# Optimization experiments

Hardware: AMD Instinct MI355X
Metric: run time of the kernel (lower is better)

## Reference

```python
import jax, jax.numpy as jnp
import numpy as np

B, M, S, D, Q, H = 8, 8192, 128, 512, 32, 8
HD = D // H
LN_EPS = 1e-5


def setup_inputs() -> dict:
    key = jax.random.key(0)
    ks = jax.random.split(key, 12)
    inp = {
        "memory": jax.random.normal(ks[0], (B, M, D), dtype=jnp.float32),
        "context": jax.random.normal(ks[1], (B, S, D), dtype=jnp.float32),
        "memory_mask": jax.random.randint(ks[2], (B, M), 0, 2).astype(bool),
        # learned parameters
        "queries_param": jax.random.normal(ks[3], (Q, D), dtype=jnp.float32) * 0.02,
        "ctx_w": jax.random.normal(ks[4], (D, D), dtype=jnp.float32) / np.sqrt(D),
        "ctx_b": jnp.zeros((D,), dtype=jnp.float32),
        "in_w": jax.random.normal(ks[5], (3 * D, D), dtype=jnp.float32) / np.sqrt(D),
        "in_b": jnp.zeros((3 * D,), dtype=jnp.float32),
        "out_w": jax.random.normal(ks[6], (D, D), dtype=jnp.float32) / np.sqrt(D),
        "out_b": jnp.zeros((D,), dtype=jnp.float32),
        "ln_g": jnp.ones((D,), dtype=jnp.float32),
        "ln_b": jnp.zeros((D,), dtype=jnp.float32),
        "gate_w": jax.random.normal(ks[7], (Q, D), dtype=jnp.float32) / np.sqrt(D),
        "gate_b": jnp.zeros((Q,), dtype=jnp.float32),
    }
    return inp


def _forward(memory, context, memory_mask, queries_param, ctx_w, ctx_b,
             in_w, in_b, out_w, out_b, ln_g, ln_b, gate_w, gate_b):
    b = memory.shape[0]
    # pool context over sequence dim (rank-3 path)
    pooled = context.mean(axis=1)  # [B, D]
    # queries + projected context
    queries = queries_param[None, :, :] + (pooled @ ctx_w.T + ctx_b)[:, None, :]  # [B, Q, D]
    # MultiheadAttention in-projection
    wq, wk, wv = in_w[:D], in_w[D:2 * D], in_w[2 * D:]
    bq, bk, bv = in_b[:D], in_b[D:2 * D], in_b[2 * D:]
    qh = (queries @ wq.T + bq).reshape(b, Q, H, HD).transpose(0, 2, 1, 3)   # [B,H,Q,hd]
    kh = (memory @ wk.T + bk).reshape(b, M, H, HD).transpose(0, 2, 1, 3)    # [B,H,M,hd]
    vh = (memory @ wv.T + bv).reshape(b, M, H, HD).transpose(0, 2, 1, 3)    # [B,H,M,hd]
    scale = 1.0 / np.sqrt(HD)
    scores = jnp.einsum('bhqd,bhkd->bhqk', qh * scale, kh)                  # [B,H,Q,M]
    # key_padding_mask: True in memory_mask means valid; invalid -> -inf
    scores = jnp.where(memory_mask[:, None, None, :], scores, -jnp.inf)
    attn = jax.nn.softmax(scores, axis=-1)                                   # [B,H,Q,M]
    ctx_out = jnp.einsum('bhqk,bhkd->bhqd', attn, vh)
    ctx_out = ctx_out.transpose(0, 2, 1, 3).reshape(b, Q, D)
    readouts = ctx_out @ out_w.T + out_b                                     # [B,Q,D]
    attention = attn.mean(axis=1)                                            # [B,Q,M]
    gates = jax.nn.sigmoid(pooled @ gate_w.T + gate_b)                       # [B,Q]
    readouts = readouts * gates[:, :, None]
    mu = readouts.mean(axis=-1, keepdims=True)
    var = readouts.var(axis=-1, keepdims=True)
    readouts_norm = (readouts - mu) * jax.lax.rsqrt(var + LN_EPS) * ln_g + ln_b
    return readouts_norm, attention, gates, queries


def reference(memory, context, memory_mask, queries_param, ctx_w, ctx_b,
              in_w, in_b, out_w, out_b, ln_g, ln_b, gate_w, gate_b):
    return _forward(memory, context, memory_mask, queries_param, ctx_w, ctx_b,
                    in_w, in_b, out_w, out_b, ln_g, ln_b, gate_w, gate_b)
```

## Files before the change

kernel.cpp:

```cpp
#include <hip/hip_runtime.h>
#include <cstdint>

#define BB 8
#define MM 8192
#define SS 128
#define DD 512
#define QQ 32
#define HH 8
#define HDD 64
#define LN_EPS 1e-5f

typedef __bf16 bf16;
typedef _Float16 f16;
typedef __attribute__((ext_vector_type(8))) __bf16 bf16x8;
typedef __attribute__((ext_vector_type(4))) __bf16 bf16x4;
typedef __attribute__((ext_vector_type(8))) _Float16 f16x8;
typedef __attribute__((ext_vector_type(4))) float f32x4;

#define NEG_INF (-__builtin_inff())

__global__ __launch_bounds__(512) void k_front(const float* __restrict__ ctx,
                                               const float* __restrict__ ctx_w,
                                               const float* __restrict__ ctx_b,
                                               const float* __restrict__ qp,
                                               const float* __restrict__ gate_w,
                                               const float* __restrict__ gate_b,
                                               float* __restrict__ q_out,
                                               float* __restrict__ gates_out) {
    __shared__ float pl[DD];
    __shared__ float scratch[512];
    __shared__ float proj[64];
    int blk = blockIdx.x;
    int b = blk >> 3, js = blk & 7;
    int t = threadIdx.x;
    const float* p = ctx + (size_t)b * SS * DD + t;
    float s = 0.f;
#pragma unroll 8
    for (int i = 0; i < SS; i++) s += p[(size_t)i * DD];
    pl[t] = s * (1.0f / SS);
    __syncthreads();
    int r = js * 64 + (t & 63), ks = t >> 6;
    {
        const f32x4* wr = (const f32x4*)(ctx_w + (size_t)r * DD + ks * 64);
        const f32x4* pv = (const f32x4*)(pl + ks * 64);
        float a = 0.f;
#pragma unroll
        for (int k = 0; k < 16; k++) {
            f32x4 w = wr[k], pp = pv[k];
            a += w.x * pp.x + w.y * pp.y + w.z * pp.z + w.w * pp.w;
        }
        scratch[t] = a;
    }
    __syncthreads();
    if (t < 64) {
        float sum = ctx_b[js * 64 + t];
#pragma unroll
        for (int s8 = 0; s8 < 8; s8++) sum += scratch[t + 64 * s8];
        proj[t] = sum;
    }
    __syncthreads();
    int col = js * 64 + (t & 63);
    float pr = proj[t & 63];
#pragma unroll
    for (int qq = 0; qq < 4; qq++) {
        int q = (t >> 6) * 4 + qq;
        q_out[((size_t)(b * QQ + q)) * DD + col] = qp[q * DD + col] + pr;
    }
    if (js == 0 && t < QQ) {
        const f32x4* gw = (const f32x4*)(gate_w + (size_t)t * DD);
        const f32x4* pv = (const f32x4*)pl;
        float ga = 0.f;
#pragma unroll 8
        for (int k = 0; k < DD / 4; k++) {
            f32x4 w = gw[k], pp = pv[k];
            ga += w.x * pp.x + w.y * pp.y + w.z * pp.z + w.w * pp.w;
        }
        gates_out[b * QQ + t] = 1.0f / (1.0f + __expf(-(ga + gate_b[t])));
    }
}

__global__ __launch_bounds__(256) void k_qh(const float* __restrict__ q_in,
                                            const float* __restrict__ in_w,
                                            const float* __restrict__ in_b,
                                            float* __restrict__ qh) {
    __shared__ float qr[QQ * DD];
    int blk = blockIdx.x;
    int b = blk >> 3, js = blk & 7;
    int t = threadIdx.x;
    const f32x4* src = (const f32x4*)(q_in + (size_t)b * QQ * DD);
    f32x4* dst = (f32x4*)qr;
    for (int i = t; i < QQ * DD / 4; i += 256) dst[i] = src[i];
    __syncthreads();
    int j = js * 64 + (t & 63);
    int qg = t >> 6;
    const f32x4* wv = (const f32x4*)(in_w + (size_t)j * DD);
    float acc[8];
#pragma unroll
    for (int e = 0; e < 8; e++) acc[e] = 0.f;
    for (int k = 0; k < DD / 4; k++) {
        f32x4 w = wv[k];
#pragma unroll
        for (int e = 0; e < 8; e++) {
            f32x4 qq = ((const f32x4*)qr)[(qg * 8 + e) * (DD / 4) + k];
            acc[e] += w.x * qq.x + w.y * qq.y + w.z * qq.z + w.w * qq.w;
        }
    }
    float bias = in_b[j];
#pragma unroll
    for (int e = 0; e < 8; e++) {
        int q = qg * 8 + e;
        qh[((size_t)(b * QQ + q)) * DD + j] = 0.125f * (acc[e] + bias);
    }
}

#define N4_MEM 8388608
#define N4_W   131072
__global__ __launch_bounds__(256) void k_cvt2(const float* __restrict__ mem,
                                              const float* __restrict__ wsrc,
                                              bf16* __restrict__ memB,
                                              bf16* __restrict__ kvwB) {
    int stride = gridDim.x * blockDim.x;
    for (int i = blockIdx.x * blockDim.x + threadIdx.x; i < N4_MEM + N4_W; i += stride) {
        if (i < N4_MEM) {
            f32x4 v = ((const f32x4*)mem)[i];
            bf16x4 o;
            o.x = (bf16)v.x; o.y = (bf16)v.y; o.z = (bf16)v.z; o.w = (bf16)v.w;
            ((bf16x4*)memB)[i] = o;
        } else {
            int j = i - N4_MEM;
            f32x4 v = ((const f32x4*)wsrc)[j];
            bf16x4 o;
            o.x = (bf16)v.x; o.y = (bf16)v.y; o.z = (bf16)v.z; o.w = (bf16)v.w;
            ((bf16x4*)kvwB)[j] = o;
        }
    }
}

#define GLOAD(gp, lp)                                                                   \
    __builtin_amdgcn_global_load_lds((const __attribute__((address_space(1))) void*)(gp), \
                                     (__attribute__((address_space(3))) void*)(lp), 16, 0, 0)

__global__ __launch_bounds__(512, 2) void k_gemm_kv(const bf16* __restrict__ A,
                                                    const bf16* __restrict__ Bw,
                                                    const float* __restrict__ in_b,
                                                    bf16* __restrict__ Kh,
                                                    f16* __restrict__ Vt) {
    __shared__ __align__(16) bf16 sm[65536];
    const int tid = threadIdx.x;
    const int w = tid >> 6, l = tid & 63;
    const int wm = w >> 2, wn = w & 3;
    const int lq = l & 15, quad = l >> 4, lx = l & 7;
    const int lr = l >> 3, gc = (l & 7) ^ lr;
    const int sb = (w >> 1) * 8 + (w & 1) * 2;

    const int bid = blockIdx.x;
    const int swz = (bid & 7) * 128 + (bid >> 3);
    const int bm = swz >> 2, bn = swz & 3;

    const bf16* aPtr = A + (size_t)(bm * 256 + w * 8 + lr) * 512 + gc * 8;
    const bf16* bPtr = Bw + (size_t)(bn * 256 + sb * 8 + lr) * 512 + gc * 8;

#pragma unroll
    for (int p = 0; p < 4; p++) GLOAD(aPtr + p * 32768, sm + (p * 8 + w) * 512);
#pragma unroll
    for (int p = 0; p < 4; p++) {
        GLOAD(bPtr + ((p & 1) * 8 + (p >> 1) * 32) * 512,
              sm + 16384 + (sb + (p & 1) + (p >> 1) * 4) * 512);
        if (p == 1) __builtin_amdgcn_sched_barrier(0);
    }
    aPtr += 64;
    bPtr += 64;

    const f32x4 vzero = {0.f, 0.f, 0.f, 0.f};
    f32x4 acc[8][4];
#pragma unroll
    for (int i = 0; i < 8; i++)
#pragma unroll
        for (int j = 0; j < 4; j++) acc[i][j] = vzero;

#pragma unroll
    for (int T = 0; T < 8; T++) {
        bf16* Ab = sm + (T & 1) * 32768;
        bf16* Bb = Ab + 16384;
        bf16* AbN = sm + ((T + 1) & 1) * 32768;
        bf16* BbN = AbN + 16384;
        const bool pf = (T < 7);

        asm volatile("s_waitcnt vmcnt(2)" ::: "memory");
        __builtin_amdgcn_s_barrier();
        bf16x8 af[8][2], b01[2][2];
        {
            const int c0 = (quad ^ lx) << 3;
#pragma unroll
            for (int i = 0; i < 8; i++) {
                const bf16* rp = Ab + (wm * 128 + i * 16 + lq) * 64;
                af[i][0] = *(const bf16x8*)(rp + c0);
                af[i][1] = *(const bf16x8*)(rp + (c0 ^ 32));
            }
#pragma unroll
            for (int j = 0; j < 2; j++) {
                const bf16* rp = Bb + (wn * 64 + j * 16 + lq) * 64;
                b01[j][0] = *(const bf16x8*)(rp + c0);
                b01[j][1] = *(const bf16x8*)(rp + (c0 ^ 32));
            }
        }
        if (pf) {
#pragma unroll
            for (int p = 0; p < 4; p++) GLOAD(aPtr + p * 32768, AbN + (p * 8 + w) * 512);
            aPtr += 64;
        }
        __builtin_amdgcn_s_setprio(1);
#pragma unroll
        for (int i = 0; i < 8; i++)
#pragma unroll
            for (int j = 0; j < 2; j++) {
                acc[i][j] = __builtin_amdgcn_mfma_f32_16x16x32_bf16(af[i][0], b01[j][0], acc[i][j], 0, 0, 0);
                acc[i][j] = __builtin_amdgcn_mfma_f32_16x16x32_bf16(af[i][1], b01[j][1], acc[i][j], 0, 0, 0);
            }
        __builtin_amdgcn_s_setprio(0);

        if (pf) {
            asm volatile("s_waitcnt vmcnt(4)" ::: "memory");
        } else {
            asm volatile("s_waitcnt vmcnt(0)" ::: "memory");
        }
        __builtin_amdgcn_s_barrier();
        bf16x8 b23[2][2];
        {
            const int c0 = (quad ^ lx) << 3;
#pragma unroll
            for (int j = 0; j < 2; j++) {
                const bf16* rp = Bb + (wn * 64 + 32 + j * 16 + lq) * 64;
                b23[j][0] = *(const bf16x8*)(rp + c0);
                b23[j][1] = *(const bf16x8*)(rp + (c0 ^ 32));
            }
        }
        if (pf) {
#pragma unroll
            for (int p = 0; p < 4; p++) {
                GLOAD(bPtr + ((p & 1) * 8 + (p >> 1) * 32) * 512,
                      BbN + (sb + (p & 1) + (p >> 1) * 4) * 512);
                if (p == 1) __builtin_amdgcn_sched_barrier(0);
            }
            bPtr += 64;
        }
        __builtin_amdgcn_s_setprio(1);
#pragma unroll
        for (int i = 0; i < 8; i++)
#pragma unroll
            for (int j = 0; j < 2; j++) {
                acc[i][2 + j] = __builtin_amdgcn_mfma_f32_16x16x32_bf16(af[i][0], b23[j][0], acc[i][2 + j], 0, 0, 0);
                acc[i][2 + j] = __builtin_amdgcn_mfma_f32_16x16x32_bf16(af[i][1], b23[j][1], acc[i][2 + j], 0, 0, 0);
            }
        __builtin_amdgcn_s_setprio(0);
    }

    __syncthreads();
    const int qn_w = wn >> 1;
    bf16* qt = sm + (((wm << 1) | qn_w) * 16384);
    const bool isV = (bn >= 2);
    if (!isV) {
#pragma unroll
        for (int j = 0; j < 4; j++) {
            int cq = (wn & 1) * 64 + j * 16 + lq;
            float bias = in_b[512 + bn * 256 + qn_w * 128 + cq];
            int cc = cq >> 3, cl = cq & 7;
#pragma unroll
            for (int i = 0; i < 8; i++) {
                int rb = i * 16 + quad * 4;
#pragma unroll
                for (int t = 0; t < 4; t++) {
                    int r = rb + t;
                    qt[r * 128 + (((cc ^ (r & 15)) << 3) | cl)] = (bf16)(acc[i][j][t] + bias);
                }
            }
        }
        __syncthreads();
        for (int idx = tid; idx < 8192; idx += 512) {
            int qq2 = idx >> 11;
            int rr = (idx >> 4) & 127, ch2 = idx & 15;
            bf16x8 v = *(const bf16x8*)(sm + qq2 * 16384 + rr * 128 + ((ch2 ^ (rr & 15)) << 3));
            int m = bm * 256 + (qq2 >> 1) * 128 + rr;
            int cg = bn * 256 + (qq2 & 1) * 128 + ch2 * 8;
            int b = m >> 13, mloc = m & 8191;
            int h = cg >> 6, d = cg & 63;
            *(bf16x8*)(Kh + (((size_t)(b * 8 + h) * 8192 + mloc) << 6) + d) = v;
        }
    } else {
        f16* qth = (f16*)qt;
#pragma unroll
        for (int j = 0; j < 4; j++) {
            int cq = (wn & 1) * 64 + j * 16 + lq;
            float bias = in_b[512 + bn * 256 + qn_w * 128 + cq];
            int cs = cq & 15;
#pragma unroll
            for (int i = 0; i < 8; i++) {
                int rb = i * 16 + quad * 4;
#pragma unroll
                for (int t = 0; t < 4; t++) {
                    int r = rb + t;
                    qth[cq * 128 + ((((r >> 3) ^ cs) << 3) | (r & 7))] = (f16)(acc[i][j][t] + bias);
                }
            }
        }
        __syncthreads();
        for (int idx = tid; idx < 8192; idx += 512) {
            int qq2 = idx >> 11;
            int cq = (idx >> 4) & 127, ch2 = idx & 15;
            f16x8 v = *(const f16x8*)((const f16*)sm + qq2 * 16384 + cq * 128 + ((ch2 ^ (cq & 15)) << 3));
            int hd = (bn - 2) * 256 + (qq2 & 1) * 128 + cq;
            int m = bm * 256 + (qq2 >> 1) * 128 + ch2 * 8;
            int b = m >> 13, mloc = m & 8191;
            *(f16x8*)(Vt + ((size_t)(b * 512 + hd)) * MM + mloc) = v;
        }
    }
}
#undef GLOAD

__global__ __launch_bounds__(256) void k_scores(const float* __restrict__ qh,
                                                const bf16* __restrict__ kvK,
                                                const f16* __restrict__ Vt,
                                                const int* __restrict__ mask,
                                                f16* __restrict__ s16,
                                                float* __restrict__ statsM,
                                                float* __restrict__ statsS,
                                                float* __restrict__ cp) {
    __shared__ __align__(16) f16 tile[QQ * 520];
    __shared__ float ctile[QQ * HDD];
    __shared__ float smx[QQ][4];
    __shared__ float sse[QQ][4];
    __shared__ float qmax[QQ];
    int blk = blockIdx.x;
    int mt = blk & 15, h = (blk >> 4) & 7, b = blk >> 7;
    int tid = threadIdx.x, w = tid >> 6, l = tid & 63;
    int lq = l & 15, quad = l >> 4;
    int mbase = mt * 512 + w * 128;

    for (int i = tid; i < QQ * HDD; i += 256) ctile[i] = 0.f;

    bf16x8 af[2][2];
#pragma unroll
    for (int i = 0; i < 2; i++)
#pragma unroll
        for (int s = 0; s < 2; s++) {
            const float* qp = qh + ((size_t)(b * QQ + i * 16 + lq)) * DD + h * 64 + s * 32 + quad * 8;
            f32x4 q0 = *(const f32x4*)qp;
            f32x4 q1 = *(const f32x4*)(qp + 4);
            bf16x8 v;
            v[0] = (bf16)q0.x; v[1] = (bf16)q0.y; v[2] = (bf16)q0.z; v[3] = (bf16)q0.w;
            v[4] = (bf16)q1.x; v[5] = (bf16)q1.y; v[6] = (bf16)q1.z; v[7] = (bf16)q1.w;
            af[i][s] = v;
        }

    const f32x4 vzero = {0.f, 0.f, 0.f, 0.f};
    f32x4 acc[2][8];
#pragma unroll
    for (int i = 0; i < 2; i++)
#pragma unroll
        for (int n = 0; n < 8; n++) acc[i][n] = vzero;

#pragma unroll
    for (int n = 0; n < 8; n++) {
        int m = mbase + n * 16 + lq;
        const bf16* kp = kvK + (((size_t)(b * HH + h) * MM + m) << 6) + quad * 8;
        bf16x8 b0 = *(const bf16x8*)kp;
        bf16x8 b1 = *(const bf16x8*)(kp + 32);
#pragma unroll
        for (int i = 0; i < 2; i++) {
            acc[i][n] = __builtin_amdgcn_mfma_f32_16x16x32_bf16(af[i][0], b0, acc[i][n], 0, 0, 0);
            acc[i][n] = __builtin_amdgcn_mfma_f32_16x16x32_bf16(af[i][1], b1, acc[i][n], 0, 0, 0);
        }
    }
#pragma unroll
    for (int n = 0; n < 8; n++) {
        int mv = mask[b * MM + mbase + n * 16 + lq];
        if (!mv) {
#pragma unroll
            for (int i = 0; i < 2; i++)
#pragma unroll
                for (int t = 0; t < 4; t++) acc[i][n][t] = NEG_INF;
        }
    }
    float mx[2][4];
#pragma unroll
    for (int i = 0; i < 2; i++)
#pragma unroll
        for (int t = 0; t < 4; t++) {
            float m = acc[i][0][t];
#pragma unroll
            for (int n = 1; n < 8; n++) m = fmaxf(m, acc[i][n][t]);
            mx[i][t] = m;
        }
#pragma unroll
    for (int off = 1; off < 16; off <<= 1)
#pragma unroll
        for (int i = 0; i < 2; i++)
#pragma unroll
            for (int t = 0; t < 4; t++) mx[i][t] = fmaxf(mx[i][t], __shfl_xor(mx[i][t], off, 64));
    if (lq == 0) {
#pragma unroll
        for (int i = 0; i < 2; i++)
#pragma unroll
            for (int t = 0; t < 4; t++) smx[i * 16 + quad * 4 + t][w] = mx[i][t];
    }
    __syncthreads();
    if (tid < QQ) qmax[tid] = fmaxf(fmaxf(smx[tid][0], smx[tid][1]), fmaxf(smx[tid][2], smx[tid][3]));
    __syncthreads();
    float se[2][4];
#pragma unroll
    for (int i = 0; i < 2; i++)
#pragma unroll
        for (int t = 0; t < 4; t++) {
            int qrow = i * 16 + quad * 4 + t;
            float qm = qmax[qrow];
            float s = 0.f;
#pragma unroll
            for (int n = 0; n < 8; n++) {
                float p = __expf(acc[i][n][t] - qm);
                s += p;
                tile[qrow * 520 + w * 128 + n * 16 + lq] = (f16)p;
            }
            se[i][t] = s;
        }
#pragma unroll
    for (int off = 1; off < 16; off <<= 1)
#pragma unroll
        for (int i = 0; i < 2; i++)
#pragma unroll
            for (int t = 0; t < 4; t++) se[i][t] += __shfl_xor(se[i][t], off, 64);
    if (lq == 0) {
#pragma unroll
        for (int i = 0; i < 2; i++)
#pragma unroll
            for (int t = 0; t < 4; t++) sse[i * 16 + quad * 4 + t][w] = se[i][t];
    }
    __syncthreads();
    if (tid < QQ) {
        statsM[(size_t)blk * QQ + tid] = qmax[tid];
        statsS[(size_t)blk * QQ + tid] = sse[tid][0] + sse[tid][1] + sse[tid][2] + sse[tid][3];
    }
    for (int it = tid; it < 2048; it += 256) {
        int q = it >> 6, c = it & 63;
        f16x8 v = *(const f16x8*)(tile + q * 520 + c * 8);
        *(f16x8*)(s16 + ((size_t)((b * HH + h) * QQ + q)) * MM + mt * 512 + c * 8) = v;
    }
    f32x4 acc2[2][4];
#pragma unroll
    for (int i = 0; i < 2; i++)
#pragma unroll
        for (int j = 0; j < 4; j++) acc2[i][j] = vzero;
    const f16* vbase = Vt + ((size_t)(b * 512 + h * 64 + lq)) * MM + mbase + quad * 8;
#pragma unroll
    for (int ks = 0; ks < 4; ks++) {
        f16x8 pb[2];
        pb[0] = *(const f16x8*)(tile + lq * 520 + w * 128 + ks * 32 + quad * 8);
        pb[1] = *(const f16x8*)(tile + (16 + lq) * 520 + w * 128 + ks * 32 + quad * 8);
        f16x8 va[4];
#pragma unroll
        for (int j = 0; j < 4; j++)
            va[j] = *(const f16x8*)(vbase + (size_t)(j * 16) * MM + ks * 32);
#pragma unroll
        for (int j = 0; j < 4; j++) {
            acc2[0][j] = __builtin_amdgcn_mfma_f32_16x16x32_f16(va[j], pb[0], acc2[0][j], 0, 0, 0);
            acc2[1][j] = __builtin_amdgcn_mfma_f32_16x16x32_f16(va[j], pb[1], acc2[1][j], 0, 0, 0);
        }
    }
#pragma unroll
    for (int i = 0; i < 2; i++)
#pragma unroll
        for (int j = 0; j < 4; j++)
#pragma unroll
            for (int t = 0; t < 4; t++)
                atomicAdd(&ctile[(i * 16 + lq) * HDD + j * 16 + quad * 4 + t], acc2[i][j][t]);
    __syncthreads();
    {
        f32x4* cd = (f32x4*)(cp + ((size_t)((b * HH + h) * 16 + mt)) * (QQ * HDD));
        const f32x4* cs = (const f32x4*)ctile;
        for (int i = tid; i < QQ * HDD / 4; i += 256) cd[i] = cs[i];
    }
}

__global__ __launch_bounds__(256) void k_outln(const float* __restrict__ cp,
                                               const float* __restrict__ statsM,
                                               const float* __restrict__ statsS,
                                               const f16* __restrict__ s16,
                                               const float* __restrict__ out_w,
                                               const float* __restrict__ out_b,
                                               const float* __restrict__ gates,
                                               const float* __restrict__ ln_g,
                                               const float* __restrict__ ln_b,
                                               float* __restrict__ out0,
                                               float* __restrict__ attn_out) {
    __shared__ float cr[DD];
    __shared__ float cM[128], cS[128], sMh[8], siL[8], wgt[128];
    __shared__ float sred[4], sred2[4];
    int bq = blockIdx.x, t = threadIdx.x;
    int b = bq >> 5, q = bq & 31;
    if (t < 128) {
        int h = t >> 4, c = t & 15;
        size_t sidx = (size_t)(((b * HH + h) * 16 + c)) * QQ + q;
        cM[t] = statsM[sidx];
        cS[t] = statsS[sidx];
    }
    __syncthreads();
    if (t < 8) {
        float M = NEG_INF;
#pragma unroll
        for (int c = 0; c < 16; c++) M = fmaxf(M, cM[t * 16 + c]);
        float L = 0.f;
#pragma unroll
        for (int c = 0; c < 16; c++) L += cS[t * 16 + c] * __expf(cM[t * 16 + c] - M);
        sMh[t] = M;
        siL[t] = 1.0f / L;
    }
    __syncthreads();
    if (t < 128) wgt[t] = __expf(cM[t] - sMh[t >> 4]) * siL[t >> 4];
    __syncthreads();
    int h0 = t >> 6, h1 = h0 + 4;
    int dl = t & 63;
    const float* cp0 = cp + ((size_t)((b * HH + h0) * 16)) * (QQ * HDD) + q * HDD + dl;
    const float* cp1 = cp + ((size_t)((b * HH + h1) * 16)) * (QQ * HDD) + q * HDD + dl;
    float c0 = 0.f, c1 = 0.f;
#pragma unroll
    for (int c = 0; c < 16; c++) {
        c0 += cp0[(size_t)c * (QQ * HDD)] * wgt[h0 * 16 + c];
        c1 += cp1[(size_t)c * (QQ * HDD)] * wgt[h1 * 16 + c];
    }
    cr[t] = c0;
    cr[t + 256] = c1;
    __syncthreads();
    float g = gates[bq];
    const f32x4* cv = (const f32x4*)cr;
    float r[2];
#pragma unroll
    for (int jj = 0; jj < 2; jj++) {
        int j = t + jj * 256;
        const f32x4* wv = (const f32x4*)(out_w + (size_t)j * DD);
        float acc = 0.f;
#pragma unroll 4
        for (int k = 0; k < DD / 4; k++) {
            f32x4 wq = wv[k], cq = cv[k];
            acc += wq.x * cq.x + wq.y * cq.y + wq.z * cq.z + wq.w * cq.w;
        }
        r[jj] = (acc + out_b[j]) * g;
    }
    float s1 = r[0] + r[1];
    float s2 = r[0] * r[0] + r[1] * r[1];
    for (int off = 32; off; off >>= 1) {
        s1 += __shfl_xor(s1, off, 64);
        s2 += __shfl_xor(s2, off, 64);
    }
    int wid = t >> 6;
    if ((t & 63) == 0) { sred[wid] = s1; sred2[wid] = s2; }
    __syncthreads();
    float S1 = sred[0] + sred[1] + sred[2] + sred[3];
    float S2 = sred2[0] + sred2[1] + sred2[2] + sred2[3];
    float mu = S1 * (1.0f / DD);
    float var = S2 * (1.0f / DD) - mu * mu;
    float rs = rsqrtf(var + LN_EPS);
#pragma unroll
    for (int jj = 0; jj < 2; jj++) {
        int j = t + jj * 256;
        out0[(size_t)bq * DD + j] = (r[jj] - mu) * rs * ln_g[j] + ln_b[j];
    }
#pragma unroll
    for (int ms = 0; ms < 4; ms++) {
        int m0 = ms * 2048 + t * 8;
        int cloc = ms * 4 + (t >> 6);
        float am[8];
#pragma unroll
        for (int e = 0; e < 8; e++) am[e] = 0.f;
#pragma unroll
        for (int h = 0; h < HH; h++) {
            f16x8 v = *(const f16x8*)(s16 + ((size_t)((b * HH + h) * QQ + q)) * MM + m0);
            float wc = wgt[h * 16 + cloc];
#pragma unroll
            for (int e = 0; e < 8; e++) am[e] += (float)v[e] * wc;
        }
        float* ao = attn_out + (size_t)bq * MM + m0;
        f32x4 o0 = {am[0] * 0.125f, am[1] * 0.125f, am[2] * 0.125f, am[3] * 0.125f};
        f32x4 o1 = {am[4] * 0.125f, am[5] * 0.125f, am[6] * 0.125f, am[7] * 0.125f};
        *(f32x4*)ao = o0;
        *(f32x4*)(ao + 4) = o1;
    }
}

extern "C" void kernel_launch(void* const* d_in, const int* in_sizes, int n_in,
                              void* d_out, int out_size, void* d_ws, size_t ws_size,
                              hipStream_t stream) {
    const float* memory  = (const float*)d_in[0];
    const float* context = (const float*)d_in[1];
    const int*   mask    = (const int*)d_in[2];
    const float* qp      = (const float*)d_in[3];
    const float* ctx_w   = (const float*)d_in[4];
    const float* ctx_b   = (const float*)d_in[5];
    const float* in_w    = (const float*)d_in[6];
    const float* in_b    = (const float*)d_in[7];
    const float* out_w   = (const float*)d_in[8];
    const float* out_b   = (const float*)d_in[9];
    const float* ln_g    = (const float*)d_in[10];
    const float* ln_b    = (const float*)d_in[11];
    const float* gate_w  = (const float*)d_in[12];
    const float* gate_b  = (const float*)d_in[13];

    float* out       = (float*)d_out;
    float* out_ln    = out;
    float* out_attn  = out + 131072;
    float* out_gates = out + 131072 + 2097152;
    float* out_q     = out_gates + 256;

    char* ws = (char*)d_ws;
    bf16*  memB   = (bf16*)ws;
    f16*   s16    = (f16*)ws;
    float* cp     = (float*)(ws + 35651584);
    bf16*  kvK    = (bf16*)(ws + 67108864);
    f16*   Vt     = (f16*)(ws + 134217728);
    bf16*  kvwB   = (bf16*)(ws + 201326592);
    float* statsM = (float*)(ws + 201588736);
    float* statsS = (float*)(ws + 201719808);
    float* qh     = (float*)(ws + 202375168);

    k_front<<<64, 512, 0, stream>>>(context, ctx_w, ctx_b, qp, gate_w, gate_b, out_q, out_gates);
    k_qh<<<64, 256, 0, stream>>>(out_q, in_w, in_b, qh);
    k_cvt2<<<2048, 256, 0, stream>>>(memory, in_w + 262144, memB, kvwB);
    k_gemm_kv<<<1024, 512, 0, stream>>>(memB, kvwB, in_b, kvK, Vt);
    k_scores<<<1024, 256, 0, stream>>>(qh, kvK, Vt, mask, s16, statsM, statsS, cp);
    k_outln<<<BB * QQ, 256, 0, stream>>>(cp, statsM, statsS, s16, out_w, out_b, out_gates,
                                         ln_g, ln_b, out_ln, out_attn);
}
```

Measured before the change: 479.1 us.

## Compact valid memory rows via mask prefix-sum and skip masked work

```diff
diff --git a/kernel.cpp b/kernel.cpp
--- a/kernel.cpp
+++ b/kernel.cpp
@@ -18,6 +18,44 @@
 typedef __attribute__((ext_vector_type(4))) float f32x4;
 
 #define NEG_INF (-__builtin_inff())
+
+__global__ __launch_bounds__(256) void k_mask(const int* __restrict__ mask,
+                                              int* __restrict__ midx,
+                                              int* __restrict__ pos,
+                                              int* __restrict__ mv) {
+    __shared__ int wsum[4];
+    __shared__ int base;
+    int b = blockIdx.x, t = threadIdx.x;
+    int lane = t & 63, w = t >> 6;
+    if (t == 0) base = 0;
+    __syncthreads();
+    for (int pass = 0; pass < 32; pass++) {
+        int m = pass * 256 + t;
+        int v = mask[b * MM + m] ? 1 : 0;
+        unsigned long long ball = __ballot(v != 0);
+        int excl = __popcll(ball & ((1ULL << lane) - 1ULL));
+        if (lane == 0) wsum[w] = __popcll(ball);
+        __syncthreads();
+        int woff = 0;
+#pragma unroll
+        for (int k = 0; k < 4; k++) woff += (k < w) ? wsum[k] : 0;
+        int total = wsum[0] + wsum[1] + wsum[2] + wsum[3];
+        int j = base + woff + excl;
+        if (v) {
+            midx[b * MM + j] = m;
+            pos[b * MM + m] = j;
+        } else {
+            pos[b * MM + m] = -1;
+        }
+        __syncthreads();
+        if (t == 0) base += total;
+        __syncthreads();
+    }
+    if (t == 0) {
+        mv[b] = base;
+        mv[8 + b] = (base + 511) & ~511;
+    }
+}
 
 __global__ __launch_bounds__(512) void k_front(const float* __restrict__ ctx,
                                                const float* __restrict__ ctx_w,
@@ -113,25 +151,37 @@
     }
 }
 
-#define N4_MEM 8388608
-#define N4_W   131072
-__global__ __launch_bounds__(256) void k_cvt2(const float* __restrict__ mem,
-                                              const float* __restrict__ wsrc,
-                                              bf16* __restrict__ memB,
-                                              bf16* __restrict__ kvwB) {
-    int stride = gridDim.x * blockDim.x;
-    for (int i = blockIdx.x * blockDim.x + threadIdx.x; i < N4_MEM + N4_W; i += stride) {
-        if (i < N4_MEM) {
-            f32x4 v = ((const f32x4*)mem)[i];
+__global__ __launch_bounds__(256) void k_gather(const float* __restrict__ memf,
+                                                const float* __restrict__ wsrc,
+                                                const int* __restrict__ midx,
+                                                const int* __restrict__ mv,
+                                                bf16* __restrict__ memB,
+                                                bf16* __restrict__ kvwB) {
+    int blk = blockIdx.x, t = threadIdx.x;
+    if (blk < 2016) {
+        int w = t >> 6, lane = t & 63;
+        for (int s = blk * 4 + w; s < BB * MM; s += 2016 * 4) {
+            int b = s >> 13, j = s & 8191;
+            if (j >= mv[8 + b]) continue;
+            bf16x8 o;
+            if (j < mv[b]) {
+                int src = midx[b * MM + j];
+                const f32x4* sp = (const f32x4*)(memf + ((size_t)(b * MM + src)) * DD + lane * 8);
+                f32x4 v0 = sp[0], v1 = sp[1];
+                o[0] = (bf16)v0.x; o[1] = (bf16)v0.y; o[2] = (bf16)v0.z; o[3] = (bf16)v0.w;
+                o[4] = (bf16)v1.x; o[5] = (bf16)v1.y; o[6] = (bf16)v1.z; o[7] = (bf16)v1.w;
+            } else {
+#pragma unroll
+                for (int e = 0; e < 8; e++) o[e] = (bf16)0.0f;
+            }
+            *(bf16x8*)(memB + ((size_t)(b * MM + j)) * DD + lane * 8) = o;
+        }
+    } else {
+        for (int i = (blk - 2016) * 256 + t; i < 131072; i += 32 * 256) {
+            f32x4 v = ((const f32x4*)wsrc)[i];
             bf16x4 o;
             o.x = (bf16)v.x; o.y = (bf16)v.y; o.z = (bf16)v.z; o.w = (bf16)v.w;
-            ((bf16x4*)memB)[i] = o;
-        } else {
-            int j = i - N4_MEM;
-            f32x4 v = ((const f32x4*)wsrc)[j];
-            bf16x4 o;
-            o.x = (bf16)v.x; o.y = (bf16)v.y; o.z = (bf16)v.z; o.w = (bf16)v.w;
-            ((bf16x4*)kvwB)[j] = o;
+            ((bf16x4*)kvwB)[i] = o;
         }
     }
 }
@@ -143,6 +193,7 @@
 __global__ __launch_bounds__(512, 2) void k_gemm_kv(const bf16* __restrict__ A,
                                                     const bf16* __restrict__ Bw,
                                                     const float* __restrict__ in_b,
+                                                    const int* __restrict__ mv,
                                                     bf16* __restrict__ Kh,
                                                     f16* __restrict__ Vt) {
     __shared__ __align__(16) bf16 sm[65536];
@@ -156,6 +207,8 @@
     const int bid = blockIdx.x;
     const int swz = (bid & 7) * 128 + (bid >> 3);
     const int bm = swz >> 2, bn = swz & 3;
+
+    if (((bm & 31) * 256) >= mv[8 + (bm >> 5)]) return;
 
     const bf16* aPtr = A + (size_t)(bm * 256 + w * 8 + lr) * 512 + gc * 8;
     const bf16* bPtr = Bw + (size_t)(bn * 256 + sb * 8 + lr) * 512 + gc * 8;
@@ -320,7 +373,7 @@
 __global__ __launch_bounds__(256) void k_scores(const float* __restrict__ qh,
                                                 const bf16* __restrict__ kvK,
                                                 const f16* __restrict__ Vt,
-                                                const int* __restrict__ mask,
+                                                const int* __restrict__ mv,
                                                 f16* __restrict__ s16,
                                                 float* __restrict__ statsM,
                                                 float* __restrict__ statsS,
@@ -334,6 +387,14 @@
     int mt = blk & 15, h = (blk >> 4) & 7, b = blk >> 7;
     int tid = threadIdx.x, w = tid >> 6, l = tid & 63;
     int lq = l & 15, quad = l >> 4;
+    int Mvb = mv[b];
+    if (mt * 512 >= Mvb) {
+        if (tid < QQ) {
+            statsM[(size_t)blk * QQ + tid] = NEG_INF;
+            statsS[(size_t)blk * QQ + tid] = 0.f;
+        }
+        return;
+    }
     int mbase = mt * 512 + w * 128;
 
     for (int i = tid; i < QQ * HDD; i += 256) ctile[i] = 0.f;
@@ -373,8 +434,7 @@
     }
 #pragma unroll
     for (int n = 0; n < 8; n++) {
-        int mv = mask[b * MM + mbase + n * 16 + lq];
-        if (!mv) {
+        if (mbase + n * 16 + lq >= Mvb) {
 #pragma unroll
             for (int i = 0; i < 2; i++)
 #pragma unroll
@@ -484,18 +544,20 @@
                                                const float* __restrict__ statsM,
                                                const float* __restrict__ statsS,
                                                const f16* __restrict__ s16,
+                                               const int* __restrict__ mv,
                                                const float* __restrict__ out_w,
                                                const float* __restrict__ out_b,
                                                const float* __restrict__ gates,
                                                const float* __restrict__ ln_g,
                                                const float* __restrict__ ln_b,
                                                float* __restrict__ out0,
-                                               float* __restrict__ attn_out) {
+                                               float* __restrict__ tmpA) {
     __shared__ float cr[DD];
     __shared__ float cM[128], cS[128], sMh[8], siL[8], wgt[128];
     __shared__ float sred[4], sred2[4];
     int bq = blockIdx.x, t = threadIdx.x;
     int b = bq >> 5, q = bq & 31;
+    int Mvb = mv[b];
     if (t < 128) {
         int h = t >> 4, c = t & 15;
         size_t sidx = (size_t)(((b * HH + h) * 16 + c)) * QQ + q;
@@ -509,12 +571,13 @@
         for (int c = 0; c < 16; c++) M = fmaxf(M, cM[t * 16 + c]);
         float L = 0.f;
 #pragma unroll
-        for (int c = 0; c < 16; c++) L += cS[t * 16 + c] * __expf(cM[t * 16 + c] - M);
+        for (int c = 0; c < 16; c++)
+            if (cS[t * 16 + c] > 0.f) L += cS[t * 16 + c] * __expf(cM[t * 16 + c] - M);
         sMh[t] = M;
         siL[t] = 1.0f / L;
     }
     __syncthreads();
-    if (t < 128) wgt[t] = __expf(cM[t] - sMh[t >> 4]) * siL[t >> 4];
+    if (t < 128) wgt[t] = (cS[t] > 0.f) ? __expf(cM[t] - sMh[t >> 4]) * siL[t >> 4] : 0.f;
     __syncthreads();
     int h0 = t >> 6, h1 = h0 + 4;
     int dl = t & 63;
@@ -523,8 +586,9 @@
     float c0 = 0.f, c1 = 0.f;
 #pragma unroll
     for (int c = 0; c < 16; c++) {
-        c0 += cp0[(size_t)c * (QQ * HDD)] * wgt[h0 * 16 + c];
-        c1 += cp1[(size_t)c * (QQ * HDD)] * wgt[h1 * 16 + c];
+        float w0 = wgt[h0 * 16 + c], w1 = wgt[h1 * 16 + c];
+        if (w0 > 0.f) c0 += cp0[(size_t)c * (QQ * HDD)] * w0;
+        if (w1 > 0.f) c1 += cp1[(size_t)c * (QQ * HDD)] * w1;
     }
     cr[t] = c0;
     cr[t + 256] = c1;
@@ -565,24 +629,42 @@
     }
 #pragma unroll
     for (int ms = 0; ms < 4; ms++) {
-        int m0 = ms * 2048 + t * 8;
-        int cloc = ms * 4 + (t >> 6);
+        int j0 = ms * 2048 + t * 8;
+        if (j0 >= Mvb) continue;
+        int cloc = j0 >> 9;
         float am[8];
 #pragma unroll
         for (int e = 0; e < 8; e++) am[e] = 0.f;
 #pragma unroll
         for (int h = 0; h < HH; h++) {
-            f16x8 v = *(const f16x8*)(s16 + ((size_t)((b * HH + h) * QQ + q)) * MM + m0);
+            f16x8 v = *(const f16x8*)(s16 + ((size_t)((b * HH + h) * QQ + q)) * MM + j0);
             float wc = wgt[h * 16 + cloc];
 #pragma unroll
             for (int e = 0; e < 8; e++) am[e] += (float)v[e] * wc;
         }
-        float* ao = attn_out + (size_t)bq * MM + m0;
+        float* ao = tmpA + (size_t)bq * MM + j0;
         f32x4 o0 = {am[0] * 0.125f, am[1] * 0.125f, am[2] * 0.125f, am[3] * 0.125f};
         f32x4 o1 = {am[4] * 0.125f, am[5] * 0.125f, am[6] * 0.125f, am[7] * 0.125f};
         *(f32x4*)ao = o0;
         *(f32x4*)(ao + 4) = o1;
     }
+}
+
+__global__ __launch_bounds__(256) void k_scatter(const float* __restrict__ tmpA,
+                                                 const int* __restrict__ pos,
+                                                 float* __restrict__ attn_out) {
+    int idx = blockIdx.x * 256 + threadIdx.x;
+    int L = idx * 4;
+    int bq = L >> 13, m = L & 8191;
+    int b = bq >> 5;
+    int4 p4 = *(const int4*)(pos + b * MM + m);
+    const float* tb_ = tmpA + (size_t)bq * MM;
+    f32x4 o;
+    o.x = (p4.x >= 0) ? tb_[p4.x] : 0.f;
+    o.y = (p4.y >= 0) ? tb_[p4.y] : 0.f;
+    o.z = (p4.z >= 0) ? tb_[p4.z] : 0.f;
+    o.w = (p4.w >= 0) ? tb_[p4.w] : 0.f;
+    *(f32x4*)(attn_out + (size_t)bq * MM + m) = o;
 }
 
 extern "C" void kernel_launch(void* const* d_in, const int* in_sizes, int n_in,
@@ -613,18 +695,24 @@
     bf16*  memB   = (bf16*)ws;
     f16*   s16    = (f16*)ws;
     float* cp     = (float*)(ws + 35651584);
+    float* tmpA   = (float*)(ws + 44040192);
     bf16*  kvK    = (bf16*)(ws + 67108864);
     f16*   Vt     = (f16*)(ws + 134217728);
     bf16*  kvwB   = (bf16*)(ws + 201326592);
     float* statsM = (float*)(ws + 201588736);
     float* statsS = (float*)(ws + 201719808);
     float* qh     = (float*)(ws + 202375168);
-
+    int*   midx   = (int*)(ws + 202899456);
+    int*   pos    = (int*)(ws + 203161600);
+    int*   mv     = (int*)(ws + 203423744);
+
+    k_mask<<<8, 256, 0, stream>>>(mask, midx, pos, mv);
     k_front<<<64, 512, 0, stream>>>(context, ctx_w, ctx_b, qp, gate_w, gate_b, out_q, out_gates);
     k_qh<<<64, 256, 0, stream>>>(out_q, in_w, in_b, qh);
-    k_cvt2<<<2048, 256, 0, stream>>>(memory, in_w + 262144, memB, kvwB);
-    k_gemm_kv<<<1024, 512, 0, stream>>>(memB, kvwB, in_b, kvK, Vt);
-    k_scores<<<1024, 256, 0, stream>>>(qh, kvK, Vt, mask, s16, statsM, statsS, cp);
-    k_outln<<<BB * QQ, 256, 0, stream>>>(cp, statsM, statsS, s16, out_w, out_b, out_gates,
-                                         ln_g, ln_b, out_ln, out_attn);
-}
+    k_gather<<<2048, 256, 0, stream>>>(memory, in_w + 262144, midx, mv, memB, kvwB);
+    k_gemm_kv<<<1024, 512, 0, stream>>>(memB, kvwB, in_b, mv, kvK, Vt);
+    k_scores<<<1024, 256, 0, stream>>>(qh, kvK, Vt, mv, s16, statsM, statsS, cp);
+    k_outln<<<BB * QQ, 256, 0, stream>>>(cp, statsM, statsS, s16, mv, out_w, out_b, out_gates,
+                                         ln_g, ln_b, out_ln, tmpA);
+    k_scatter<<<2048, 256, 0, stream>>>(tmpA, pos, out_attn);
+}
```

Measured after the change: 460.1 us. 1.04x faster.
